# Kernel optimization log

Hardware: AMD Instinct MI355X
Metric: run time of the kernel (lower is better)

The kernel has to match this reference:

```python
import jax, jax.numpy as jnp
import numpy as np

NUM_NODES = 50000
FEAT_DIM = 256
CLIPS = 8
DIM = 128
K_NEIGH = 32
B, S = 2048, 10


def setup_inputs() -> dict:
    key = jax.random.key(0)
    k1, k2, k3, k4 = jax.random.split(key, 4)
    nodes = jax.random.randint(k1, (B, S), 0, NUM_NODES, dtype=jnp.int64)
    adj = jax.random.randint(k2, (NUM_NODES, K_NEIGH), 0, NUM_NODES, dtype=jnp.int64)
    features = jax.random.normal(k3, (NUM_NODES, FEAT_DIM), dtype=jnp.float32)
    # xavier-uniform-ish scale for local_weight [clips, dim, feat_dim]
    limit = float(np.sqrt(6.0 / (DIM + FEAT_DIM)))
    local_weight = jax.random.uniform(k4, (CLIPS, DIM, FEAT_DIM), dtype=jnp.float32,
                                      minval=-limit, maxval=limit)
    return {"nodes": nodes, "adj": adj, "features": features, "local_weight": local_weight}


def reference(nodes, adj, features, local_weight):
    # order == 1: one hop of mean aggregation over sampled neighbor lists
    nodes_flat = nodes.reshape(-1)                      # [n]
    neigh = adj[nodes_flat]                             # [n, K] irregular gather
    feat = features[neigh].mean(axis=1)                 # [n, d] gather + mean
    # einsum('ckd,dn->ckn').permute(2,0,1) == einsum('ckd,nd->nck')
    local_out = jnp.einsum('ckd,nd->nck', local_weight, feat)   # [n, clips, dim]
    local_embs = jax.nn.relu(local_out)
    return local_embs.reshape(nodes.shape[0], nodes.shape[1], local_weight.shape[0], -1)
```

## Files before the change

kernel.cpp:

```cpp
#include <hip/hip_runtime.h>

#define FEAT_DIM 256
#define K_NEIGH  32
#define NROWS    20480
#define NOUT     1024
#define NUM_NODES 50000
#define SLICE_DIM 32
#define NSLICE    8

typedef __attribute__((ext_vector_type(8))) short bf16x8;
typedef __attribute__((ext_vector_type(4))) float f32x4;

__device__ __forceinline__ unsigned short f2bf(float f) {
    unsigned int u = __builtin_bit_cast(unsigned int, f);
    u += 0x7fffu + ((u >> 16) & 1u);
    return (unsigned short)(u >> 16);
}
__device__ __forceinline__ float bf2f(unsigned short h) {
    unsigned int u = ((unsigned int)h) << 16;
    return __builtin_bit_cast(float, u);
}
__device__ __forceinline__ void gload16(const void* g, void* l) {
    __builtin_amdgcn_global_load_lds(
        (const __attribute__((address_space(1))) unsigned int*)g,
        (__attribute__((address_space(3))) unsigned int*)l, 16, 0, 0);
}

__global__ __launch_bounds__(256) void wcvt_kernel(const float* __restrict__ w,
                                                   unsigned short* __restrict__ wb) {
    int i = (blockIdx.x * 256 + threadIdx.x) * 4;
    float4 v = *(const float4*)(w + i);
    ushort4 o;
    o.x = f2bf(v.x); o.y = f2bf(v.y); o.z = f2bf(v.z); o.w = f2bf(v.w);
    *(ushort4*)(wb + i) = o;
}

__global__ __launch_bounds__(256) void fcvt_sliced(const float* __restrict__ f,
                                                   unsigned short* __restrict__ fb) {
    int t = threadIdx.x;
    int node = blockIdx.x * 16 + (t >> 4);
    int part = t & 15;
    int slice = part >> 1, half = part & 1;
    const float* src = f + (long)node * FEAT_DIM + part * 16;
    unsigned short o[16];
    #pragma unroll
    for (int j = 0; j < 16; j += 4) {
        float4 v = *(const float4*)(src + j);
        o[j] = f2bf(v.x); o[j+1] = f2bf(v.y); o[j+2] = f2bf(v.z); o[j+3] = f2bf(v.w);
    }
    unsigned short* dst = fb + ((long)slice * NUM_NODES + node) * SLICE_DIM + half * 16;
    *(bf16x8*)dst = *(const bf16x8*)o;
    *(bf16x8*)(dst + 8) = *(const bf16x8*)(o + 8);
}

__global__ __launch_bounds__(256) void agg_sliced(const int* __restrict__ nodes,
                                                  const int* __restrict__ adj,
                                                  const unsigned short* __restrict__ fb,
                                                  unsigned short* __restrict__ feat) {
    int slice = blockIdx.x & 7;
    int chunk = blockIdx.x >> 3;
    int t = threadIdx.x;
    int row = chunk * 64 + (t >> 2);
    int d8 = (t & 3) * 8;
    int node = nodes[row];
    const int* arow = adj + (long)node * K_NEIGH;
    int nbr[K_NEIGH];
    #pragma unroll
    for (int kk = 0; kk < K_NEIGH / 4; ++kk)
        *(int4*)(nbr + kk * 4) = ((const int4*)arow)[kk];

    const unsigned short* base = fb + (long)slice * NUM_NODES * SLICE_DIM + d8;
    float acc[8] = {};
    #pragma unroll
    for (int k = 0; k < K_NEIGH; ++k) {
        bf16x8 v = *(const bf16x8*)(base + (long)nbr[k] * SLICE_DIM);
        #pragma unroll
        for (int j = 0; j < 8; ++j) acc[j] += bf2f((unsigned short)v[j]);
    }
    unsigned short o[8];
    #pragma unroll
    for (int j = 0; j < 8; ++j) o[j] = f2bf(acc[j] * (1.0f / K_NEIGH));
    *(bf16x8*)(feat + (long)row * FEAT_DIM + slice * SLICE_DIM + d8) = *(const bf16x8*)o;
}

__global__ __launch_bounds__(256) void agg_f32_kernel(const int* __restrict__ nodes,
                                                      const int* __restrict__ adj,
                                                      const float* __restrict__ features,
                                                      unsigned short* __restrict__ feat) {
    int row = blockIdx.x;
    int t = threadIdx.x;
    int node = nodes[row];
    const int* arow = adj + (long)node * K_NEIGH;
    float acc = 0.f;
    #pragma unroll
    for (int k = 0; k < K_NEIGH; ++k) {
        long nb = arow[k];
        acc += features[nb * FEAT_DIM + t];
    }
    feat[(long)row * FEAT_DIM + t] = f2bf(acc * (1.0f / K_NEIGH));
}

__global__ __launch_bounds__(256) void gemm_kernel(const unsigned short* __restrict__ A,
                                                   const unsigned short* __restrict__ Bw,
                                                   float* __restrict__ C) {
    __shared__ short As[128 * 32];
    __shared__ short Bs[128 * 32];

    int t = threadIdx.x;
    int wave = t >> 6, lane = t & 63;
    int wm = wave >> 1, wn = wave & 1;
    int m0 = blockIdx.x * 128, n0 = blockIdx.y * 128;
    int lr = lane & 15;
    int lk = (lane >> 4) * 8;

    int srow = t >> 2;
    int sseg = (t & 3) * 8;
    const short* Ag = (const short*)A + (long)(m0 + srow) * FEAT_DIM + sseg;
    const short* Bg = (const short*)Bw + (long)(n0 + srow) * FEAT_DIM + sseg;
    short* Al = As + t * 8;
    short* Bl = Bs + t * 8;

    f32x4 acc[4][4] = {};

    for (int kb = 0; kb < FEAT_DIM; kb += 32) {
        if (kb) __syncthreads();
        gload16(Ag + kb, Al);
        gload16(Ag + 64 * FEAT_DIM + kb, Al + 64 * 32);
        gload16(Bg + kb, Bl);
        gload16(Bg + 64 * FEAT_DIM + kb, Bl + 64 * 32);
        __syncthreads();

        bf16x8 a[4], b[4];
        #pragma unroll
        for (int i = 0; i < 4; ++i)
            a[i] = *(const bf16x8*)(As + (wm * 64 + i * 16 + lr) * 32 + lk);
        #pragma unroll
        for (int j = 0; j < 4; ++j)
            b[j] = *(const bf16x8*)(Bs + (wn * 64 + j * 16 + lr) * 32 + lk);
        #pragma unroll
        for (int i = 0; i < 4; ++i)
            #pragma unroll
            for (int j = 0; j < 4; ++j)
                acc[i][j] = __builtin_amdgcn_mfma_f32_16x16x32_bf16(a[i], b[j], acc[i][j], 0, 0, 0);
    }

    int crow0 = m0 + wm * 64 + (lane >> 4) * 4;
    int ccol0 = n0 + wn * 64 + lr;
    #pragma unroll
    for (int i = 0; i < 4; ++i)
        #pragma unroll
        for (int j = 0; j < 4; ++j)
            #pragma unroll
            for (int r = 0; r < 4; ++r) {
                float v = acc[i][j][r];
                C[(long)(crow0 + i * 16 + r) * NOUT + ccol0 + j * 16] = v > 0.f ? v : 0.f;
            }
}

extern "C" void kernel_launch(void* const* d_in, const int* in_sizes, int n_in,
                              void* d_out, int out_size, void* d_ws, size_t ws_size,
                              hipStream_t stream) {
    const int*   nodes    = (const int*)d_in[0];
    const int*   adj      = (const int*)d_in[1];
    const float* features = (const float*)d_in[2];
    const float* lw       = (const float*)d_in[3];
    float*       out      = (float*)d_out;

    const size_t fbf_elems  = (size_t)NUM_NODES * FEAT_DIM;
    const size_t feat_elems = (size_t)NROWS * FEAT_DIM;
    const size_t need = (fbf_elems + feat_elems + (size_t)NOUT * FEAT_DIM) * 2;

    if (ws_size >= need) {
        unsigned short* fbf  = (unsigned short*)d_ws;
        unsigned short* feat = fbf + fbf_elems;
        unsigned short* wb   = feat + feat_elems;

        wcvt_kernel<<<(NOUT * FEAT_DIM) / (256 * 4), 256, 0, stream>>>(lw, wb);
        fcvt_sliced<<<NUM_NODES / 16, 256, 0, stream>>>(features, fbf);
        agg_sliced<<<(NROWS / 64) * NSLICE, 256, 0, stream>>>(nodes, adj, fbf, feat);
        gemm_kernel<<<dim3(NROWS / 128, NOUT / 128), 256, 0, stream>>>(feat, wb, out);
    } else {
        unsigned short* feat = (unsigned short*)d_ws;
        unsigned short* wb   = feat + feat_elems;

        wcvt_kernel<<<(NOUT * FEAT_DIM) / (256 * 4), 256, 0, stream>>>(lw, wb);
        agg_f32_kernel<<<NROWS, 256, 0, stream>>>(nodes, adj, features, feat);
        gemm_kernel<<<dim3(NROWS / 128, NOUT / 128), 256, 0, stream>>>(feat, wb, out);
    }
}
```

Before: 78.27 us.

## Merge conversion kernels and double-buffer GEMM LDS staging

Folds the weight and feature bf16 conversion kernels into one launch, removing a kernel launch. The feature conversion is remapped so each thread converts a full 32-element slice, with adjacent lanes handling adjacent nodes. The GEMM now double-buffers its LDS tiles, prefetching the next K-step while MFMAs run on the current one, so only one barrier per step is needed. This doubles the GEMM's LDS use, and the new conversion mapping makes each lane's float4 loads stride across separate rows, which may coalesce worse.

```diff
diff --git a/kernel.cpp b/kernel.cpp
--- a/kernel.cpp
+++ b/kernel.cpp
@@ -7,6 +7,7 @@
 #define NUM_NODES 50000
 #define SLICE_DIM 32
 #define NSLICE    8
+#define FBLK      1563
 
 typedef __attribute__((ext_vector_type(8))) short bf16x8;
 typedef __attribute__((ext_vector_type(4))) float f32x4;
@@ -35,22 +36,35 @@
     *(ushort4*)(wb + i) = o;
 }
 
-__global__ __launch_bounds__(256) void fcvt_sliced(const float* __restrict__ f,
-                                                   unsigned short* __restrict__ fb) {
-    int t = threadIdx.x;
-    int node = blockIdx.x * 16 + (t >> 4);
-    int part = t & 15;
-    int slice = part >> 1, half = part & 1;
-    const float* src = f + (long)node * FEAT_DIM + part * 16;
-    unsigned short o[16];
-    #pragma unroll
-    for (int j = 0; j < 16; j += 4) {
-        float4 v = *(const float4*)(src + j);
-        o[j] = f2bf(v.x); o[j+1] = f2bf(v.y); o[j+2] = f2bf(v.z); o[j+3] = f2bf(v.w);
-    }
-    unsigned short* dst = fb + ((long)slice * NUM_NODES + node) * SLICE_DIM + half * 16;
-    *(bf16x8*)dst = *(const bf16x8*)o;
-    *(bf16x8*)(dst + 8) = *(const bf16x8*)(o + 8);
+__global__ __launch_bounds__(256) void cvt_kernel(const float* __restrict__ f,
+                                                  unsigned short* __restrict__ fb,
+                                                  const float* __restrict__ w,
+                                                  unsigned short* __restrict__ wb) {
+    int b = blockIdx.x;
+    int t = threadIdx.x;
+    if (b < FBLK) {
+        int g = t >> 5;
+        int i = t & 31;
+        int node = b * 32 + i;
+        if (node >= NUM_NODES) return;
+        const float* src = f + (long)node * FEAT_DIM + g * SLICE_DIM;
+        unsigned short o[32];
+        #pragma unroll
+        for (int j = 0; j < 32; j += 4) {
+            float4 v = *(const float4*)(src + j);
+            o[j] = f2bf(v.x); o[j+1] = f2bf(v.y); o[j+2] = f2bf(v.z); o[j+3] = f2bf(v.w);
+        }
+        unsigned short* dst = fb + ((long)g * NUM_NODES + node) * SLICE_DIM;
+        #pragma unroll
+        for (int j = 0; j < 4; ++j)
+            *(bf16x8*)(dst + j * 8) = *(const bf16x8*)(o + j * 8);
+    } else {
+        int i = ((b - FBLK) * 256 + t) * 4;
+        float4 v = *(const float4*)(w + i);
+        ushort4 o;
+        o.x = f2bf(v.x); o.y = f2bf(v.y); o.z = f2bf(v.z); o.w = f2bf(v.w);
+        *(ushort4*)(wb + i) = o;
+    }
 }
 
 __global__ __launch_bounds__(256) void agg_sliced(const int* __restrict__ nodes,
@@ -103,8 +117,8 @@
 __global__ __launch_bounds__(256) void gemm_kernel(const unsigned short* __restrict__ A,
                                                    const unsigned short* __restrict__ Bw,
                                                    float* __restrict__ C) {
-    __shared__ short As[128 * 32];
-    __shared__ short Bs[128 * 32];
+    __shared__ short As[2][128 * 32];
+    __shared__ short Bs[2][128 * 32];
 
     int t = threadIdx.x;
     int wave = t >> 6, lane = t & 63;
@@ -117,32 +131,44 @@
     int sseg = (t & 3) * 8;
     const short* Ag = (const short*)A + (long)(m0 + srow) * FEAT_DIM + sseg;
     const short* Bg = (const short*)Bw + (long)(n0 + srow) * FEAT_DIM + sseg;
-    short* Al = As + t * 8;
-    short* Bl = Bs + t * 8;
 
     f32x4 acc[4][4] = {};
 
-    for (int kb = 0; kb < FEAT_DIM; kb += 32) {
-        if (kb) __syncthreads();
-        gload16(Ag + kb, Al);
-        gload16(Ag + 64 * FEAT_DIM + kb, Al + 64 * 32);
-        gload16(Bg + kb, Bl);
-        gload16(Bg + 64 * FEAT_DIM + kb, Bl + 64 * 32);
-        __syncthreads();
+#define STAGE(bufi, kb) do {                                         \
+    gload16(Ag + (kb), &As[bufi][t * 8]);                            \
+    gload16(Ag + 64 * FEAT_DIM + (kb), &As[bufi][64 * 32 + t * 8]);  \
+    gload16(Bg + (kb), &Bs[bufi][t * 8]);                            \
+    gload16(Bg + 64 * FEAT_DIM + (kb), &Bs[bufi][64 * 32 + t * 8]);  \
+} while (0)
+
+    STAGE(0, 0);
+    asm volatile("s_waitcnt vmcnt(0)" ::: "memory");
+    __builtin_amdgcn_s_barrier();
+
+    #pragma unroll
+    for (int it = 0; it < 8; ++it) {
+        int cur = it & 1;
+        if (it < 7) STAGE(cur ^ 1, (it + 1) * 32);
 
         bf16x8 a[4], b[4];
         #pragma unroll
         for (int i = 0; i < 4; ++i)
-            a[i] = *(const bf16x8*)(As + (wm * 64 + i * 16 + lr) * 32 + lk);
+            a[i] = *(const bf16x8*)(&As[cur][(wm * 64 + i * 16 + lr) * 32 + lk]);
         #pragma unroll
         for (int j = 0; j < 4; ++j)
-            b[j] = *(const bf16x8*)(Bs + (wn * 64 + j * 16 + lr) * 32 + lk);
+            b[j] = *(const bf16x8*)(&Bs[cur][(wn * 64 + j * 16 + lr) * 32 + lk]);
         #pragma unroll
         for (int i = 0; i < 4; ++i)
             #pragma unroll
             for (int j = 0; j < 4; ++j)
                 acc[i][j] = __builtin_amdgcn_mfma_f32_16x16x32_bf16(a[i], b[j], acc[i][j], 0, 0, 0);
-    }
+
+        if (it < 7) {
+            asm volatile("s_waitcnt vmcnt(0)" ::: "memory");
+            __builtin_amdgcn_s_barrier();
+        }
+    }
+#undef STAGE
 
     int crow0 = m0 + wm * 64 + (lane >> 4) * 4;
     int ccol0 = n0 + wn * 64 + lr;
@@ -175,8 +201,7 @@
         unsigned short* feat = fbf + fbf_elems;
         unsigned short* wb   = feat + feat_elems;
 
-        wcvt_kernel<<<(NOUT * FEAT_DIM) / (256 * 4), 256, 0, stream>>>(lw, wb);
-        fcvt_sliced<<<NUM_NODES / 16, 256, 0, stream>>>(features, fbf);
+        cvt_kernel<<<FBLK + (NOUT * FEAT_DIM) / (256 * 4), 256, 0, stream>>>(features, fbf, lw, wb);
         agg_sliced<<<(NROWS / 64) * NSLICE, 256, 0, stream>>>(nodes, adj, fbf, feat);
         gemm_kernel<<<dim3(NROWS / 128, NOUT / 128), 256, 0, stream>>>(feat, wb, out);
     } else {
```

Result: no change. 78.16 us (-0.1%).
